# Optimization experiments

Measured on AMD Instinct MI355X. Metric: run time of the kernel, lower is better.

Reference implementation:

```python
import jax, jax.numpy as jnp
import numpy as np
import math

N, MA, NFS, K, RC = 4, 256, 128, 8, 5.0
HID, OUT = 256, 32


def setup_inputs() -> dict:
    key = jax.random.key(0)
    ks = jax.random.split(key, 9)
    z = jax.random.randint(ks[0], (N, MA), 0, 10)
    r = jax.random.normal(ks[1], (N, MA, 3), dtype=jnp.float32) * 3.0
    h = jax.random.normal(ks[2], (N, MA, NFS), dtype=jnp.float32)
    Wa = jax.random.normal(ks[3], (2 * NFS, 1), dtype=jnp.float32) * 0.05
    ba = jnp.zeros((1,), dtype=jnp.float32)
    Wp1 = jax.random.normal(ks[4], (2 * NFS, HID), dtype=jnp.float32) * 0.05
    bp1 = jnp.zeros((HID,), dtype=jnp.float32)
    Wp2 = jax.random.normal(ks[5], (HID, OUT), dtype=jnp.float32) * 0.05
    bp2 = jnp.zeros((OUT,), dtype=jnp.float32)
    return {"z": z, "r": r, "h": h, "Wa": Wa, "ba": ba,
            "Wp1": Wp1, "bp1": bp1, "Wp2": Wp2, "bp2": bp2}


def reference(z, r, h, Wa, ba, Wp1, bp1, Wp2, bp2):
    n, ma = z.shape
    nfs = h.shape[2]
    # distance vectors dv[b,i,j] = r[b,j] - r[b,i]  -> [n, ma, ma, 3]
    dv = r[:, None, :, :] - r[:, :, None, :]
    d = jnp.linalg.norm(dv, axis=3)                       # [n, ma, ma]
    eye = jnp.eye(ma, dtype=jnp.float32)
    # cosine cutoff, zeroed on the diagonal
    cf = 0.5 * (jnp.cos(math.pi * jnp.minimum(d, RC) / RC) + 1.0)
    cf = (cf - eye[None])[..., None]                      # [n, ma, ma, 1]
    # pair validity mask (z > -1 marks real atoms), diagonal removed
    m = (z > -1).astype(jnp.float32)                      # [n, ma]
    mask = m[:, None, :] * m[:, :, None] - eye[None]
    mask = jnp.clip(mask, 0.0)[..., None]                 # [n, ma, ma, 1]
    cf = cf * mask
    # pairwise feature tensor u = [h_i, h_j * cf]         # [n, ma, ma, 2*nfs]
    u1 = jnp.broadcast_to(h[:, :, None, :], (n, ma, ma, nfs))
    u2 = h[:, None, :, :] * cf
    u = jnp.concatenate([u1, u2], axis=3)
    # exp attention, masked, normalized over neighbor axis (dim 2)
    g = (u @ Wa + ba) * mask                              # [n, ma, ma, 1]
    g = jnp.exp(g) - (1.0 - mask)
    attention = g / jnp.clip(g.sum(axis=2, keepdims=True), 1e-8)
    # top-k neighbors per query atom
    att, index = jax.lax.top_k(attention[..., 0], K)      # [n, ma, K]
    att = att[..., None]
    # gather neighbor features and distance vectors
    h2 = jnp.take_along_axis(h[:, None, :, :], index[..., None], axis=2)  # [n, ma, K, nfs]
    h1 = jnp.broadcast_to(h[:, :, None, :], (n, ma, K, nfs))
    uk = jnp.concatenate([h1, h2], axis=3) * att          # [n, ma, K, 2*nfs]
    dvk = jnp.take_along_axis(dv, index[..., None], axis=2)               # [n, ma, K, 3]
    dvk = dvk / jnp.clip(jnp.linalg.norm(dvk, axis=3, keepdims=True), 1e-4)
    dvk = dvk[:, :, :, None, :]                           # [n, ma, K, 1, 3]
    # pool MLP then cross with unit direction vectors
    c = jax.nn.silu(uk @ Wp1 + bp1) @ Wp2 + bp2           # [n, ma, K, OUT]
    c = c[..., None] * dvk                                # [n, ma, K, OUT, 3]
    return (z, r, c)
```

## Files before the change

### kernel.cpp

```cpp
#include <hip/hip_runtime.h>
#include <hip/hip_bf16.h>
#include <math.h>

#define NB 4
#define MA 256
#define NFS 128
#define KSEL 8
#define HID 256
#define NOUT 32
#define RCUT 5.0f
#define PI_F 3.14159265358979323846f

__global__ __launch_bounds__(256) void prep_kernel(
    const int* __restrict__ z, const float* __restrict__ r,
    const float* __restrict__ h, const float* __restrict__ Wa,
    const float* __restrict__ Wp1,
    float* __restrict__ out,
    float* __restrict__ a1, float* __restrict__ a2,
    float* __restrict__ P, float* __restrict__ Q) {
  const int b = blockIdx.x;
  const int t = threadIdx.x;
  const int r0 = 4 * b;
  const int wave = t >> 6, lane = t & 63;
  const int c = t & 63, fq = t >> 6;

  __shared__ __align__(16) float hsh[4][NFS];
  __shared__ __align__(16) float psumP[4][4][HID];
  __shared__ __align__(16) float psumQ[4][4][HID];

  ((float2*)hsh)[t] = ((const float2*)(h + (size_t)r0 * NFS))[t];
  __syncthreads();

  {
    const float h0 = hsh[wave][lane], h1 = hsh[wave][lane + 64];
    float p1 = h0 * Wa[lane]       + h1 * Wa[lane + 64];
    float p2 = h0 * Wa[NFS + lane] + h1 * Wa[NFS + lane + 64];
#pragma unroll
    for (int off = 32; off > 0; off >>= 1) {
      p1 += __shfl_down(p1, off);
      p2 += __shfl_down(p2, off);
    }
    if (lane == 0) { a1[r0 + wave] = p1; a2[r0 + wave] = p2; }
  }
  if (t < 4)  out[r0 + t] = (float)z[r0 + t];
  if (t < 12) out[NB * MA + r0 * 3 + t] = r[r0 * 3 + t];

  float4 accP[4] = {make_float4(0,0,0,0), make_float4(0,0,0,0),
                    make_float4(0,0,0,0), make_float4(0,0,0,0)};
  float4 accQ[4] = {make_float4(0,0,0,0), make_float4(0,0,0,0),
                    make_float4(0,0,0,0), make_float4(0,0,0,0)};
#pragma unroll 4
  for (int ff = 0; ff < 32; ++ff) {
    const int f = fq * 32 + ff;
    const float4 wt = *(const float4*)&Wp1[(size_t)f * HID + 4 * c];
    const float4 wb = *(const float4*)&Wp1[(size_t)(f + NFS) * HID + 4 * c];
#pragma unroll
    for (int rr = 0; rr < 4; ++rr) {
      const float hv = hsh[rr][f];
      accP[rr].x = fmaf(hv, wt.x, accP[rr].x);
      accP[rr].y = fmaf(hv, wt.y, accP[rr].y);
      accP[rr].z = fmaf(hv, wt.z, accP[rr].z);
      accP[rr].w = fmaf(hv, wt.w, accP[rr].w);
      accQ[rr].x = fmaf(hv, wb.x, accQ[rr].x);
      accQ[rr].y = fmaf(hv, wb.y, accQ[rr].y);
      accQ[rr].z = fmaf(hv, wb.z, accQ[rr].z);
      accQ[rr].w = fmaf(hv, wb.w, accQ[rr].w);
    }
  }
#pragma unroll
  for (int rr = 0; rr < 4; ++rr) {
    *(float4*)&psumP[fq][rr][4 * c] = accP[rr];
    *(float4*)&psumQ[fq][rr][4 * c] = accQ[rr];
  }
  __syncthreads();

  {
    const int r2 = t >> 6, c2 = t & 63;
    float4 sP = *(const float4*)&psumP[0][r2][4 * c2];
    float4 sQ = *(const float4*)&psumQ[0][r2][4 * c2];
#pragma unroll
    for (int q = 1; q < 4; ++q) {
      const float4 pP = *(const float4*)&psumP[q][r2][4 * c2];
      const float4 pQ = *(const float4*)&psumQ[q][r2][4 * c2];
      sP.x += pP.x; sP.y += pP.y; sP.z += pP.z; sP.w += pP.w;
      sQ.x += pQ.x; sQ.y += pQ.y; sQ.z += pQ.z; sQ.w += pQ.w;
    }
    *(float4*)&P[(size_t)(r0 + r2) * HID + 4 * c2] = sP;
    *(float4*)&Q[(size_t)(r0 + r2) * HID + 4 * c2] = sQ;
  }
}

__global__ __launch_bounds__(256) void main_kernel(
    const int* __restrict__ z, const float* __restrict__ r,
    const float* __restrict__ a1g, const float* __restrict__ a2g,
    const float* __restrict__ ba,
    const float* __restrict__ Pg, const float* __restrict__ Qg,
    const float* __restrict__ bp1,
    const float* __restrict__ Wp2g, const float* __restrict__ bp2,
    float* __restrict__ out) {
  const int row = blockIdx.x;
  const int n = row >> 8;
  const int i = row & 255;
  const int tid = threadIdx.x;
  const int lane = tid & 63;
  const int wave = tid >> 6;

  __shared__ float gsh[MA];
  __shared__ __align__(16) float hid_sh[KSEL][HID];
  __shared__ float psum2[8][KSEL][NOUT];
  __shared__ float att_sh[KSEL];
  __shared__ int   idx_sh[KSEL];
  __shared__ float dvk_sh[KSEL][3];

  const int l2o = tid & 31;
  const int l2c = tid >> 5;
  float wreg[32];
#pragma unroll
  for (int j = 0; j < 32; ++j) wreg[j] = Wp2g[(size_t)(32 * l2c + j) * NOUT + l2o];

  const float rix = r[row * 3 + 0], riy = r[row * 3 + 1], riz = r[row * 3 + 2];
  {
    const int jg = n * MA + tid;
    const float dx = r[jg * 3 + 0] - rix;
    const float dy = r[jg * 3 + 1] - riy;
    const float dz = r[jg * 3 + 2] - riz;
    const float d = sqrtf(dx * dx + dy * dy + dz * dz);
    const int mi = (z[row] > -1) ? 1 : 0;
    const int mj = (z[jg] > -1) ? 1 : 0;
    const int mask = max(mi * mj - ((tid == i) ? 1 : 0), 0);
    float g = 0.0f;
    if (mask) {
      const float cf = 0.5f * (__cosf(PI_F * fminf(d, RCUT) / RCUT) + 1.0f);
      g = __expf(a1g[row] + cf * a2g[jg] + ba[0]);
    }
    gsh[tid] = g;
  }
  __syncthreads();

  if (wave == 0) {
    float v0 = gsh[lane];
    float v1 = gsh[lane + 64];
    float v2 = gsh[lane + 128];
    float v3 = gsh[lane + 192];
    float s = (v0 + v1) + (v2 + v3);
#pragma unroll
    for (int off = 32; off > 0; off >>= 1) s += __shfl_xor(s, off);
    const float rden = 1.0f / fmaxf(s, 1e-8f);
#pragma unroll
    for (int k = 0; k < KSEL; k++) {
      float bv = v0; int bi = lane;
      if (v1 > bv) { bv = v1; bi = lane + 64; }
      if (v2 > bv) { bv = v2; bi = lane + 128; }
      if (v3 > bv) { bv = v3; bi = lane + 192; }
#pragma unroll
      for (int off = 32; off > 0; off >>= 1) {
        const float ov = __shfl_xor(bv, off);
        const int oi = __shfl_xor(bi, off);
        if (ov > bv || (ov == bv && oi < bi)) { bv = ov; bi = oi; }
      }
      if (lane == 0) { idx_sh[k] = bi; att_sh[k] = bv * rden; }
      const int slot = bi >> 6, who = bi & 63;
      if (lane == who) {
        if (slot == 0) v0 = -1.0f;
        else if (slot == 1) v1 = -1.0f;
        else if (slot == 2) v2 = -1.0f;
        else v3 = -1.0f;
      }
    }
  }
  __syncthreads();

  if (tid < KSEL) {
    const int jg = n * MA + idx_sh[tid];
    const float dx = r[jg * 3 + 0] - rix;
    const float dy = r[jg * 3 + 1] - riy;
    const float dz = r[jg * 3 + 2] - riz;
    const float nrm = fmaxf(sqrtf(dx * dx + dy * dy + dz * dz), 1e-4f);
    dvk_sh[tid][0] = dx / nrm;
    dvk_sh[tid][1] = dy / nrm;
    dvk_sh[tid][2] = dz / nrm;
  }

  {
    const float pi = Pg[(size_t)row * HID + tid];
    const float bb = bp1[tid];
#pragma unroll
    for (int k = 0; k < KSEL; k++) {
      const float q = Qg[(size_t)(n * MA + idx_sh[k]) * HID + tid];
      const float x = att_sh[k] * (pi + q) + bb;
      hid_sh[k][tid] = x / (1.0f + __expf(-x));
    }
  }
  __syncthreads();

  {
    float acc[KSEL];
#pragma unroll
    for (int k = 0; k < KSEL; ++k) acc[k] = 0.0f;
#pragma unroll
    for (int k = 0; k < KSEL; ++k) {
      const float4* __restrict__ hrow = (const float4*)&hid_sh[k][32 * l2c];
#pragma unroll
      for (int j4 = 0; j4 < 8; ++j4) {
        const float4 hv = hrow[j4];
        acc[k] = fmaf(hv.x, wreg[4 * j4 + 0],
                 fmaf(hv.y, wreg[4 * j4 + 1],
                 fmaf(hv.z, wreg[4 * j4 + 2],
                 fmaf(hv.w, wreg[4 * j4 + 3], acc[k]))));
      }
    }
#pragma unroll
    for (int k = 0; k < KSEL; ++k) psum2[l2c][k][l2o] = acc[k];
  }
  __syncthreads();

  {
    const int k2 = tid >> 5;
    const int o = tid & 31;
    float s = bp2[o];
#pragma unroll
    for (int cc = 0; cc < 8; ++cc) s += psum2[cc][k2][o];
    const float dx = dvk_sh[k2][0], dy = dvk_sh[k2][1], dz = dvk_sh[k2][2];
    float* cb = out + NB * MA + NB * MA * 3 +
                ((size_t)row * KSEL + k2) * (NOUT * 3) + o * 3;
    cb[0] = s * dx;
    cb[1] = s * dy;
    cb[2] = s * dz;
  }
}

extern "C" void kernel_launch(void* const* d_in, const int* in_sizes, int n_in,
                              void* d_out, int out_size, void* d_ws, size_t ws_size,
                              hipStream_t stream) {
  const int*   z   = (const int*)d_in[0];
  const float* r   = (const float*)d_in[1];
  const float* h   = (const float*)d_in[2];
  const float* Wa  = (const float*)d_in[3];
  const float* ba  = (const float*)d_in[4];
  const float* Wp1 = (const float*)d_in[5];
  const float* bp1 = (const float*)d_in[6];
  const float* Wp2 = (const float*)d_in[7];
  const float* bp2 = (const float*)d_in[8];
  float* out = (float*)d_out;

  float* a1 = (float*)d_ws;
  float* a2 = a1 + NB * MA;
  float* P  = a2 + NB * MA;
  float* Q  = P + (size_t)NB * MA * HID;

  prep_kernel<<<NB * MA / 4, 256, 0, stream>>>(z, r, h, Wa, Wp1, out, a1, a2, P, Q);
  main_kernel<<<NB * MA, 256, 0, stream>>>(z, r, a1, a2, ba, P, Q, bp1, Wp2, bp2, out);
}
```

Baseline: 22.89 us.

## Split prep kernel P/Q halves across blocks and replicate top-k per wave

The prep kernel now launches twice as many blocks, each computing either P or Q (half the Wp1 rows), which halves per-block register accumulators and shared memory while doubling parallelism. In the main kernel every wave redundantly runs the top-k selection, keeping indices and attention weights in registers instead of shared memory, which removes a barrier and the separate dvk pass. Direction vectors are recomputed per output thread. The cost is redundant top-k work in all four waves and repeated loads of h tiles across the two half blocks.

```diff
diff --git a/kernel.cpp b/kernel.cpp
--- a/kernel.cpp
+++ b/kernel.cpp
@@ -19,19 +19,20 @@
     float* __restrict__ a1, float* __restrict__ a2,
     float* __restrict__ P, float* __restrict__ Q) {
   const int b = blockIdx.x;
+  const int half = b & 1;
+  const int rg = b >> 1;
+  const int r0 = 4 * rg;
   const int t = threadIdx.x;
-  const int r0 = 4 * b;
   const int wave = t >> 6, lane = t & 63;
   const int c = t & 63, fq = t >> 6;
 
   __shared__ __align__(16) float hsh[4][NFS];
-  __shared__ __align__(16) float psumP[4][4][HID];
-  __shared__ __align__(16) float psumQ[4][4][HID];
+  __shared__ __align__(16) float psum[4][4][HID];
 
   ((float2*)hsh)[t] = ((const float2*)(h + (size_t)r0 * NFS))[t];
   __syncthreads();
 
-  {
+  if (half == 0) {
     const float h0 = hsh[wave][lane], h1 = hsh[wave][lane + 64];
     float p1 = h0 * Wa[lane]       + h1 * Wa[lane + 64];
     float p2 = h0 * Wa[NFS + lane] + h1 * Wa[NFS + lane + 64];
@@ -41,52 +42,40 @@
       p2 += __shfl_down(p2, off);
     }
     if (lane == 0) { a1[r0 + wave] = p1; a2[r0 + wave] = p2; }
-  }
-  if (t < 4)  out[r0 + t] = (float)z[r0 + t];
-  if (t < 12) out[NB * MA + r0 * 3 + t] = r[r0 * 3 + t];
-
-  float4 accP[4] = {make_float4(0,0,0,0), make_float4(0,0,0,0),
-                    make_float4(0,0,0,0), make_float4(0,0,0,0)};
-  float4 accQ[4] = {make_float4(0,0,0,0), make_float4(0,0,0,0),
-                    make_float4(0,0,0,0), make_float4(0,0,0,0)};
+    if (t < 4)  out[r0 + t] = (float)z[r0 + t];
+    if (t < 12) out[NB * MA + r0 * 3 + t] = r[r0 * 3 + t];
+  }
+
+  const float* __restrict__ Wbase = Wp1 + (size_t)(half ? NFS : 0) * HID;
+  float4 acc[4] = {make_float4(0,0,0,0), make_float4(0,0,0,0),
+                   make_float4(0,0,0,0), make_float4(0,0,0,0)};
 #pragma unroll 4
   for (int ff = 0; ff < 32; ++ff) {
     const int f = fq * 32 + ff;
-    const float4 wt = *(const float4*)&Wp1[(size_t)f * HID + 4 * c];
-    const float4 wb = *(const float4*)&Wp1[(size_t)(f + NFS) * HID + 4 * c];
+    const float4 w = *(const float4*)&Wbase[(size_t)f * HID + 4 * c];
 #pragma unroll
     for (int rr = 0; rr < 4; ++rr) {
       const float hv = hsh[rr][f];
-      accP[rr].x = fmaf(hv, wt.x, accP[rr].x);
-      accP[rr].y = fmaf(hv, wt.y, accP[rr].y);
-      accP[rr].z = fmaf(hv, wt.z, accP[rr].z);
-      accP[rr].w = fmaf(hv, wt.w, accP[rr].w);
-      accQ[rr].x = fmaf(hv, wb.x, accQ[rr].x);
-      accQ[rr].y = fmaf(hv, wb.y, accQ[rr].y);
-      accQ[rr].z = fmaf(hv, wb.z, accQ[rr].z);
-      accQ[rr].w = fmaf(hv, wb.w, accQ[rr].w);
-    }
-  }
-#pragma unroll
-  for (int rr = 0; rr < 4; ++rr) {
-    *(float4*)&psumP[fq][rr][4 * c] = accP[rr];
-    *(float4*)&psumQ[fq][rr][4 * c] = accQ[rr];
-  }
+      acc[rr].x = fmaf(hv, w.x, acc[rr].x);
+      acc[rr].y = fmaf(hv, w.y, acc[rr].y);
+      acc[rr].z = fmaf(hv, w.z, acc[rr].z);
+      acc[rr].w = fmaf(hv, w.w, acc[rr].w);
+    }
+  }
+#pragma unroll
+  for (int rr = 0; rr < 4; ++rr) *(float4*)&psum[fq][rr][4 * c] = acc[rr];
   __syncthreads();
 
   {
     const int r2 = t >> 6, c2 = t & 63;
-    float4 sP = *(const float4*)&psumP[0][r2][4 * c2];
-    float4 sQ = *(const float4*)&psumQ[0][r2][4 * c2];
+    float4 s = *(const float4*)&psum[0][r2][4 * c2];
 #pragma unroll
     for (int q = 1; q < 4; ++q) {
-      const float4 pP = *(const float4*)&psumP[q][r2][4 * c2];
-      const float4 pQ = *(const float4*)&psumQ[q][r2][4 * c2];
-      sP.x += pP.x; sP.y += pP.y; sP.z += pP.z; sP.w += pP.w;
-      sQ.x += pQ.x; sQ.y += pQ.y; sQ.z += pQ.z; sQ.w += pQ.w;
-    }
-    *(float4*)&P[(size_t)(r0 + r2) * HID + 4 * c2] = sP;
-    *(float4*)&Q[(size_t)(r0 + r2) * HID + 4 * c2] = sQ;
+      const float4 p = *(const float4*)&psum[q][r2][4 * c2];
+      s.x += p.x; s.y += p.y; s.z += p.z; s.w += p.w;
+    }
+    float* dst = (half ? Q : P) + (size_t)(r0 + r2) * HID + 4 * c2;
+    *(float4*)dst = s;
   }
 }
 
@@ -103,14 +92,10 @@
   const int i = row & 255;
   const int tid = threadIdx.x;
   const int lane = tid & 63;
-  const int wave = tid >> 6;
 
   __shared__ float gsh[MA];
   __shared__ __align__(16) float hid_sh[KSEL][HID];
   __shared__ float psum2[8][KSEL][NOUT];
-  __shared__ float att_sh[KSEL];
-  __shared__ int   idx_sh[KSEL];
-  __shared__ float dvk_sh[KSEL][3];
 
   const int l2o = tid & 31;
   const int l2c = tid >> 5;
@@ -137,7 +122,9 @@
   }
   __syncthreads();
 
-  if (wave == 0) {
+  float att[KSEL];
+  int   idx[KSEL];
+  {
     float v0 = gsh[lane];
     float v1 = gsh[lane + 64];
     float v2 = gsh[lane + 128];
@@ -158,7 +145,8 @@
         const int oi = __shfl_xor(bi, off);
         if (ov > bv || (ov == bv && oi < bi)) { bv = ov; bi = oi; }
       }
-      if (lane == 0) { idx_sh[k] = bi; att_sh[k] = bv * rden; }
+      att[k] = bv * rden;
+      idx[k] = __builtin_amdgcn_readfirstlane(bi);
       const int slot = bi >> 6, who = bi & 63;
       if (lane == who) {
         if (slot == 0) v0 = -1.0f;
@@ -168,26 +156,14 @@
       }
     }
   }
-  __syncthreads();
-
-  if (tid < KSEL) {
-    const int jg = n * MA + idx_sh[tid];
-    const float dx = r[jg * 3 + 0] - rix;
-    const float dy = r[jg * 3 + 1] - riy;
-    const float dz = r[jg * 3 + 2] - riz;
-    const float nrm = fmaxf(sqrtf(dx * dx + dy * dy + dz * dz), 1e-4f);
-    dvk_sh[tid][0] = dx / nrm;
-    dvk_sh[tid][1] = dy / nrm;
-    dvk_sh[tid][2] = dz / nrm;
-  }
 
   {
     const float pi = Pg[(size_t)row * HID + tid];
     const float bb = bp1[tid];
 #pragma unroll
     for (int k = 0; k < KSEL; k++) {
-      const float q = Qg[(size_t)(n * MA + idx_sh[k]) * HID + tid];
-      const float x = att_sh[k] * (pi + q) + bb;
+      const float q = Qg[(size_t)(n * MA + idx[k]) * HID + tid];
+      const float x = att[k] * (pi + q) + bb;
       hid_sh[k][tid] = x / (1.0f + __expf(-x));
     }
   }
@@ -220,12 +196,16 @@
     float s = bp2[o];
 #pragma unroll
     for (int cc = 0; cc < 8; ++cc) s += psum2[cc][k2][o];
-    const float dx = dvk_sh[k2][0], dy = dvk_sh[k2][1], dz = dvk_sh[k2][2];
+    const int jg = n * MA + idx[k2];
+    const float dx = r[jg * 3 + 0] - rix;
+    const float dy = r[jg * 3 + 1] - riy;
+    const float dz = r[jg * 3 + 2] - riz;
+    const float nrm = fmaxf(sqrtf(dx * dx + dy * dy + dz * dz), 1e-4f);
     float* cb = out + NB * MA + NB * MA * 3 +
                 ((size_t)row * KSEL + k2) * (NOUT * 3) + o * 3;
-    cb[0] = s * dx;
-    cb[1] = s * dy;
-    cb[2] = s * dz;
+    cb[0] = s * (dx / nrm);
+    cb[1] = s * (dy / nrm);
+    cb[2] = s * (dz / nrm);
   }
 }
 
@@ -248,6 +228,6 @@
   float* P  = a2 + NB * MA;
   float* Q  = P + (size_t)NB * MA * HID;
 
-  prep_kernel<<<NB * MA / 4, 256, 0, stream>>>(z, r, h, Wa, Wp1, out, a1, a2, P, Q);
+  prep_kernel<<<2 * NB * MA / 4, 256, 0, stream>>>(z, r, h, Wa, Wp1, out, a1, a2, P, Q);
   main_kernel<<<NB * MA, 256, 0, stream>>>(z, r, a1, a2, ba, P, Q, bp1, Wp2, bp2, out);
 }
```

Measured after the change: 22.91 us. About the same (+0.1%).
